# Kernel optimization log

Measured on AMD Instinct MI355X. Metric: run time of the kernel, lower is better.

The kernel has to match this reference:

```python
import jax, jax.numpy as jnp
import numpy as np

M = 4096
N = 4096

def _twiddle(L):
    k = jnp.arange(L, dtype=jnp.float32)
    ang = -np.pi * k / (2.0 * L)
    return jnp.stack([jnp.cos(ang), jnp.sin(ang)], axis=-1).astype(jnp.float32)  # [L,2] = exp(-i*pi*k/(2L))

def setup_inputs() -> dict:
    key = jax.random.key(0)
    x = jax.random.normal(key, (M, N), dtype=jnp.float32)
    return {"x": x, "expkM": _twiddle(M), "expkN": _twiddle(N)}

def reference(x, expkM, expkN):
    # 2D DCT-II via Makhoul even/odd reordering + single complex FFT2 + twiddle multiply.
    # out[u,v] = sum_{m,n} x[m,n] cos(pi*u*(2m+1)/(2M)) cos(pi*v*(2n+1)/(2N))
    Mh, Nh = x.shape
    permM = jnp.concatenate([jnp.arange(0, Mh, 2), jnp.arange(Mh - 1, 0, -2)])
    permN = jnp.concatenate([jnp.arange(0, Nh, 2), jnp.arange(Nh - 1, 0, -2)])
    y = x[permM][:, permN]                       # even/odd reorder in both dims
    Y = jnp.fft.fft2(y)                          # [M,N] complex
    wM = expkM[:, 0] + 1j * expkM[:, 1]          # exp(-i*pi*u/(2M))
    wN = expkN[:, 0] + 1j * expkN[:, 1]          # exp(-i*pi*v/(2N))
    Yrev = jnp.roll(Y[::-1, :], 1, axis=0)       # Y[(M-u) % M, v]
    C = 0.5 * (wN[None, :] * Y + jnp.conj(wN)[None, :] * jnp.conj(Yrev))
    return jnp.real(wM[:, None] * C)
```

## Files before the change

kernel.cpp:

```cpp
#include <hip/hip_runtime.h>
#include <math.h>

#define NFULL 4096
#define NH    2048
#define T     256

__device__ __forceinline__ int sw(int i) { return i ^ (((i >> 4) & 7) << 1); }

__device__ __forceinline__ float2 cmul(float2 a, float2 b) {
    return make_float2(a.x * b.x - a.y * b.y, a.x * b.y + a.y * b.x);
}

__device__ __forceinline__ float2 sc(float ang) {
    float s, c;
    __sincosf(ang, &s, &c);
    return make_float2(c, s);
}

__device__ __forceinline__ void dft8(float2 v[8]) {
    const float s = 0.70710678118654752f;
    float2 e0 = v[0], o0 = v[1], e1 = v[2], o1 = v[3];
    float2 e2 = v[4], o2 = v[5], e3 = v[6], o3 = v[7];
    float2 t0 = make_float2(e0.x + e2.x, e0.y + e2.y);
    float2 t1 = make_float2(e0.x - e2.x, e0.y - e2.y);
    float2 t2 = make_float2(e1.x + e3.x, e1.y + e3.y);
    float2 t3 = make_float2(e1.x - e3.x, e1.y - e3.y);
    float2 E0 = make_float2(t0.x + t2.x, t0.y + t2.y);
    float2 E2 = make_float2(t0.x - t2.x, t0.y - t2.y);
    float2 E1 = make_float2(t1.x + t3.y, t1.y - t3.x);
    float2 E3 = make_float2(t1.x - t3.y, t1.y + t3.x);
    float2 u0 = make_float2(o0.x + o2.x, o0.y + o2.y);
    float2 u1 = make_float2(o0.x - o2.x, o0.y - o2.y);
    float2 u2 = make_float2(o1.x + o3.x, o1.y + o3.y);
    float2 u3 = make_float2(o1.x - o3.x, o1.y - o3.y);
    float2 O0 = make_float2(u0.x + u2.x, u0.y + u2.y);
    float2 O2 = make_float2(u0.x - u2.x, u0.y - u2.y);
    float2 O1 = make_float2(u1.x + u3.y, u1.y - u3.x);
    float2 O3 = make_float2(u1.x - u3.y, u1.y + u3.x);
    O1 = make_float2(s * (O1.x + O1.y), s * (O1.y - O1.x));
    O2 = make_float2(O2.y, -O2.x);
    O3 = make_float2(s * (O3.y - O3.x), s * (-O3.x - O3.y));
    v[0] = make_float2(E0.x + O0.x, E0.y + O0.y);
    v[4] = make_float2(E0.x - O0.x, E0.y - O0.y);
    v[1] = make_float2(E1.x + O1.x, E1.y + O1.y);
    v[5] = make_float2(E1.x - O1.x, E1.y - O1.y);
    v[2] = make_float2(E2.x + O2.x, E2.y + O2.y);
    v[6] = make_float2(E2.x - O2.x, E2.y - O2.y);
    v[3] = make_float2(E3.x + O3.x, E3.y + O3.y);
    v[7] = make_float2(E3.x - O3.x, E3.y - O3.y);
}

__device__ __forceinline__ void dft4(float2 v[4]) {
    float2 t0 = make_float2(v[0].x + v[2].x, v[0].y + v[2].y);
    float2 t1 = make_float2(v[0].x - v[2].x, v[0].y - v[2].y);
    float2 t2 = make_float2(v[1].x + v[3].x, v[1].y + v[3].y);
    float2 t3 = make_float2(v[1].x - v[3].x, v[1].y - v[3].y);
    v[0] = make_float2(t0.x + t2.x, t0.y + t2.y);
    v[2] = make_float2(t0.x - t2.x, t0.y - t2.y);
    v[1] = make_float2(t1.x + t3.y, t1.y - t3.x);
    v[3] = make_float2(t1.x - t3.y, t1.y + t3.x);
}

__global__ __launch_bounds__(T, 5) void dct_rows_rfft(const float* __restrict__ in,
                                                      const float* __restrict__ expk,
                                                      float* __restrict__ out) {
    __shared__ float2 A[NH];
    __shared__ float2 B[NH];
    const int row = blockIdx.x;
    const int t = threadIdx.x;
    const float4* __restrict__ src4 = (const float4*)(in + (size_t)row * NFULL);

    float2 v[8];
    {
        float4 f0 = src4[t];
        float4 f1 = src4[t + 256];
        float4 f2 = src4[t + 512];
        float4 f3 = src4[t + 768];
        float4 g3 = src4[1023 - t];
        float4 g2 = src4[767 - t];
        float4 g1 = src4[511 - t];
        float4 g0 = src4[255 - t];
        v[0] = make_float2(f0.x, f0.z);
        v[1] = make_float2(f1.x, f1.z);
        v[2] = make_float2(f2.x, f2.z);
        v[3] = make_float2(f3.x, f3.z);
        v[4] = make_float2(g3.w, g3.y);
        v[5] = make_float2(g2.w, g2.y);
        v[6] = make_float2(g1.w, g1.y);
        v[7] = make_float2(g0.w, g0.y);
        dft8(v);
        #pragma unroll
        for (int r = 0; r < 8; ++r) B[sw(8 * t + r)] = v[r];
    }
    __syncthreads();
    {
        #pragma unroll
        for (int r = 0; r < 8; ++r) v[r] = B[sw(t + 256 * r)];
        const float a = -(float)M_PI / 32.0f * (float)(t & 7);
        float2 w1 = sc(a), w2 = sc(2.0f * a), w4 = sc(4.0f * a);
        float2 w3 = cmul(w1, w2), w5 = cmul(w1, w4), w6 = cmul(w2, w4);
        float2 w7 = cmul(w3, w4);
        v[1] = cmul(v[1], w1); v[2] = cmul(v[2], w2); v[3] = cmul(v[3], w3);
        v[4] = cmul(v[4], w4); v[5] = cmul(v[5], w5); v[6] = cmul(v[6], w6);
        v[7] = cmul(v[7], w7);
        dft8(v);
        const int d = ((t >> 3) << 6) + (t & 7);
        #pragma unroll
        for (int r = 0; r < 8; ++r) A[sw(d + 8 * r)] = v[r];
    }
    __syncthreads();
    {
        #pragma unroll
        for (int r = 0; r < 8; ++r) v[r] = A[sw(t + 256 * r)];
        const float a = -(float)M_PI / 256.0f * (float)(t & 63);
        float2 w1 = sc(a), w2 = sc(2.0f * a), w4 = sc(4.0f * a);
        float2 w3 = cmul(w1, w2), w5 = cmul(w1, w4), w6 = cmul(w2, w4);
        float2 w7 = cmul(w3, w4);
        v[1] = cmul(v[1], w1); v[2] = cmul(v[2], w2); v[3] = cmul(v[3], w3);
        v[4] = cmul(v[4], w4); v[5] = cmul(v[5], w5); v[6] = cmul(v[6], w6);
        v[7] = cmul(v[7], w7);
        dft8(v);
        const int d = ((t >> 6) << 9) + (t & 63);
        #pragma unroll
        for (int r = 0; r < 8; ++r) B[sw(d + 64 * r)] = v[r];
    }
    __syncthreads();
    #pragma unroll
    for (int h = 0; h < 2; ++h) {
        const int j = t + 256 * h;
        float2 u[4];
        #pragma unroll
        for (int r = 0; r < 4; ++r) u[r] = B[sw(j + 512 * r)];
        const float a = -(float)M_PI / 1024.0f * (float)j;
        float2 w1 = sc(a), w2 = sc(2.0f * a);
        float2 w3 = cmul(w1, w2);
        u[1] = cmul(u[1], w1);
        u[2] = cmul(u[2], w2);
        u[3] = cmul(u[3], w3);
        dft4(u);
        #pragma unroll
        for (int r = 0; r < 4; ++r) A[sw(j + 512 * r)] = u[r];
    }
    __syncthreads();

    const float2* __restrict__ ek = (const float2*)expk;
    float* __restrict__ dst = out + (size_t)row * NFULL;
    #pragma unroll
    for (int i = 0; i < 8; ++i) {
        const int k = t + T * i;
        if (k == 0) {
            float2 z0 = A[sw(0)];
            dst[0]  = ek[0].x * (z0.x + z0.y);
            dst[NH] = ek[NH].x * (z0.x - z0.y);
        } else {
            float2 Zk = A[sw(k)];
            float2 Zr = A[sw(NH - k)];
            float2 E = make_float2(0.5f * (Zk.x + Zr.x), 0.5f * (Zk.y - Zr.y));
            float2 O = make_float2(0.5f * (Zk.y + Zr.y), 0.5f * (Zr.x - Zk.x));
            float2 uu = sc(-(float)M_PI / 2048.0f * (float)k);
            float2 Y = make_float2(E.x + uu.x * O.x - uu.y * O.y,
                                   E.y + uu.x * O.y + uu.y * O.x);
            float2 wk = ek[k];
            dst[k] = wk.x * Y.x - wk.y * Y.y;
            float2 wn = ek[NFULL - k];
            dst[NFULL - k] = wn.x * Y.x + wn.y * Y.y;
        }
    }
}

__global__ __launch_bounds__(256) void transpose4k(const float* __restrict__ in,
                                                   float* __restrict__ out) {
    __shared__ float tile[32][33];
    const int x0 = blockIdx.x * 32;
    const int y0 = blockIdx.y * 32;
    const int tx = threadIdx.x & 31;
    const int ty = threadIdx.x >> 5;

    #pragma unroll
    for (int i = 0; i < 32; i += 8)
        tile[ty + i][tx] = in[(size_t)(y0 + ty + i) * NFULL + (x0 + tx)];
    __syncthreads();
    #pragma unroll
    for (int i = 0; i < 32; i += 8)
        out[(size_t)(x0 + ty + i) * NFULL + (y0 + tx)] = tile[tx][ty + i];
}

extern "C" void kernel_launch(void* const* d_in, const int* in_sizes, int n_in,
                              void* d_out, int out_size, void* d_ws, size_t ws_size,
                              hipStream_t stream) {
    const float* x     = (const float*)d_in[0];
    const float* expkM = (const float*)d_in[1];
    const float* expkN = (const float*)d_in[2];
    float* out = (float*)d_out;
    float* ws1 = (float*)d_ws;

    dct_rows_rfft<<<NFULL, T, 0, stream>>>(x, expkN, ws1);
    transpose4k<<<dim3(128, 128), 256, 0, stream>>>(ws1, out);
    dct_rows_rfft<<<NFULL, T, 0, stream>>>(out, expkM, ws1);
    transpose4k<<<dim3(128, 128), 256, 0, stream>>>(ws1, out);
}
```

Before: 113.5 us.

## Process each DCT row with a single wavefront and drop block barriers

The row DCT kernel now assigns one 64-lane wavefront per row, with two rows per 128-thread block. Each lane handles four times as many FFT butterflies, kept in registers. All __syncthreads calls are removed, relying on wavefront-level ordering of LDS accesses. A single in-place LDS buffer per row replaces the previous A/B ping-pong, halving LDS per row. The aim is to remove barrier stalls and raise per-thread ILP, at the cost of higher register pressure. It also relies on implicit intra-wave LDS ordering with no explicit fence.

```diff
diff --git a/kernel.cpp b/kernel.cpp
--- a/kernel.cpp
+++ b/kernel.cpp
@@ -3,7 +3,8 @@
 
 #define NFULL 4096
 #define NH    2048
-#define T     256
+#define ROWS_PER_BLK 2
+#define T     (64 * ROWS_PER_BLK)
 
 __device__ __forceinline__ int sw(int i) { return i ^ (((i >> 4) & 7) << 1); }
 
@@ -61,93 +62,125 @@
     v[3] = make_float2(t1.x - t3.y, t1.y + t3.x);
 }
 
-__global__ __launch_bounds__(T, 5) void dct_rows_rfft(const float* __restrict__ in,
+__global__ __launch_bounds__(T, 2) void dct_rows_wave(const float* __restrict__ in,
                                                       const float* __restrict__ expk,
                                                       float* __restrict__ out) {
-    __shared__ float2 A[NH];
-    __shared__ float2 B[NH];
-    const int row = blockIdx.x;
-    const int t = threadIdx.x;
+    __shared__ float2 L[ROWS_PER_BLK][NH];
+    const int wave = threadIdx.x >> 6;
+    const int l    = threadIdx.x & 63;
+    const int row  = ROWS_PER_BLK * blockIdx.x + wave;
+    float2* __restrict__ A = L[wave];
     const float4* __restrict__ src4 = (const float4*)(in + (size_t)row * NFULL);
 
-    float2 v[8];
+    float2 v[4][8];
+    #pragma unroll
+    for (int i = 0; i < 4; ++i) {
+        const int b = l + 64 * i;
+        float4 f0 = src4[b];
+        float4 f1 = src4[b + 256];
+        float4 f2 = src4[b + 512];
+        float4 f3 = src4[b + 768];
+        float4 g3 = src4[1023 - b];
+        float4 g2 = src4[767 - b];
+        float4 g1 = src4[511 - b];
+        float4 g0 = src4[255 - b];
+        v[i][0] = make_float2(f0.x, f0.z);
+        v[i][1] = make_float2(f1.x, f1.z);
+        v[i][2] = make_float2(f2.x, f2.z);
+        v[i][3] = make_float2(f3.x, f3.z);
+        v[i][4] = make_float2(g3.w, g3.y);
+        v[i][5] = make_float2(g2.w, g2.y);
+        v[i][6] = make_float2(g1.w, g1.y);
+        v[i][7] = make_float2(g0.w, g0.y);
+    }
+    #pragma unroll
+    for (int i = 0; i < 4; ++i) {
+        dft8(v[i]);
+        const int b = l + 64 * i;
+        #pragma unroll
+        for (int r = 0; r < 8; ++r) A[sw(8 * b + r)] = v[i][r];
+    }
+
     {
-        float4 f0 = src4[t];
-        float4 f1 = src4[t + 256];
-        float4 f2 = src4[t + 512];
-        float4 f3 = src4[t + 768];
-        float4 g3 = src4[1023 - t];
-        float4 g2 = src4[767 - t];
-        float4 g1 = src4[511 - t];
-        float4 g0 = src4[255 - t];
-        v[0] = make_float2(f0.x, f0.z);
-        v[1] = make_float2(f1.x, f1.z);
-        v[2] = make_float2(f2.x, f2.z);
-        v[3] = make_float2(f3.x, f3.z);
-        v[4] = make_float2(g3.w, g3.y);
-        v[5] = make_float2(g2.w, g2.y);
-        v[6] = make_float2(g1.w, g1.y);
-        v[7] = make_float2(g0.w, g0.y);
-        dft8(v);
-        #pragma unroll
-        for (int r = 0; r < 8; ++r) B[sw(8 * t + r)] = v[r];
-    }
-    __syncthreads();
-    {
-        #pragma unroll
-        for (int r = 0; r < 8; ++r) v[r] = B[sw(t + 256 * r)];
-        const float a = -(float)M_PI / 32.0f * (float)(t & 7);
+        #pragma unroll
+        for (int i = 0; i < 4; ++i)
+            #pragma unroll
+            for (int r = 0; r < 8; ++r) v[i][r] = A[sw(l + 64 * i + 256 * r)];
+        const float a = -(float)M_PI / 32.0f * (float)(l & 7);
         float2 w1 = sc(a), w2 = sc(2.0f * a), w4 = sc(4.0f * a);
         float2 w3 = cmul(w1, w2), w5 = cmul(w1, w4), w6 = cmul(w2, w4);
         float2 w7 = cmul(w3, w4);
-        v[1] = cmul(v[1], w1); v[2] = cmul(v[2], w2); v[3] = cmul(v[3], w3);
-        v[4] = cmul(v[4], w4); v[5] = cmul(v[5], w5); v[6] = cmul(v[6], w6);
-        v[7] = cmul(v[7], w7);
-        dft8(v);
-        const int d = ((t >> 3) << 6) + (t & 7);
-        #pragma unroll
-        for (int r = 0; r < 8; ++r) A[sw(d + 8 * r)] = v[r];
-    }
-    __syncthreads();
+        #pragma unroll
+        for (int i = 0; i < 4; ++i) {
+            v[i][1] = cmul(v[i][1], w1); v[i][2] = cmul(v[i][2], w2);
+            v[i][3] = cmul(v[i][3], w3); v[i][4] = cmul(v[i][4], w4);
+            v[i][5] = cmul(v[i][5], w5); v[i][6] = cmul(v[i][6], w6);
+            v[i][7] = cmul(v[i][7], w7);
+            dft8(v[i]);
+        }
+        #pragma unroll
+        for (int i = 0; i < 4; ++i) {
+            const int q = l + 64 * i;
+            const int d = ((q >> 3) << 6) + (q & 7);
+            #pragma unroll
+            for (int r = 0; r < 8; ++r) A[sw(d + 8 * r)] = v[i][r];
+        }
+    }
+
     {
         #pragma unroll
-        for (int r = 0; r < 8; ++r) v[r] = A[sw(t + 256 * r)];
-        const float a = -(float)M_PI / 256.0f * (float)(t & 63);
+        for (int i = 0; i < 4; ++i)
+            #pragma unroll
+            for (int r = 0; r < 8; ++r) v[i][r] = A[sw(l + 64 * i + 256 * r)];
+        const float a = -(float)M_PI / 256.0f * (float)l;
         float2 w1 = sc(a), w2 = sc(2.0f * a), w4 = sc(4.0f * a);
         float2 w3 = cmul(w1, w2), w5 = cmul(w1, w4), w6 = cmul(w2, w4);
         float2 w7 = cmul(w3, w4);
-        v[1] = cmul(v[1], w1); v[2] = cmul(v[2], w2); v[3] = cmul(v[3], w3);
-        v[4] = cmul(v[4], w4); v[5] = cmul(v[5], w5); v[6] = cmul(v[6], w6);
-        v[7] = cmul(v[7], w7);
-        dft8(v);
-        const int d = ((t >> 6) << 9) + (t & 63);
-        #pragma unroll
-        for (int r = 0; r < 8; ++r) B[sw(d + 64 * r)] = v[r];
-    }
-    __syncthreads();
-    #pragma unroll
-    for (int h = 0; h < 2; ++h) {
-        const int j = t + 256 * h;
-        float2 u[4];
-        #pragma unroll
-        for (int r = 0; r < 4; ++r) u[r] = B[sw(j + 512 * r)];
-        const float a = -(float)M_PI / 1024.0f * (float)j;
-        float2 w1 = sc(a), w2 = sc(2.0f * a);
-        float2 w3 = cmul(w1, w2);
-        u[1] = cmul(u[1], w1);
-        u[2] = cmul(u[2], w2);
-        u[3] = cmul(u[3], w3);
-        dft4(u);
-        #pragma unroll
-        for (int r = 0; r < 4; ++r) A[sw(j + 512 * r)] = u[r];
-    }
-    __syncthreads();
+        #pragma unroll
+        for (int i = 0; i < 4; ++i) {
+            v[i][1] = cmul(v[i][1], w1); v[i][2] = cmul(v[i][2], w2);
+            v[i][3] = cmul(v[i][3], w3); v[i][4] = cmul(v[i][4], w4);
+            v[i][5] = cmul(v[i][5], w5); v[i][6] = cmul(v[i][6], w6);
+            v[i][7] = cmul(v[i][7], w7);
+            dft8(v[i]);
+        }
+        #pragma unroll
+        for (int i = 0; i < 4; ++i) {
+            const int q = l + 64 * i;
+            const int d = ((q >> 6) << 9) + (q & 63);
+            #pragma unroll
+            for (int r = 0; r < 8; ++r) A[sw(d + 64 * r)] = v[i][r];
+        }
+    }
+
+    {
+        float2 u[8][4];
+        #pragma unroll
+        for (int i = 0; i < 8; ++i)
+            #pragma unroll
+            for (int r = 0; r < 4; ++r) u[i][r] = A[sw(l + 64 * i + 512 * r)];
+        #pragma unroll
+        for (int i = 0; i < 8; ++i) {
+            const int q = l + 64 * i;
+            const float a = -(float)M_PI / 1024.0f * (float)q;
+            float2 w1 = sc(a), w2 = sc(2.0f * a);
+            float2 w3 = cmul(w1, w2);
+            u[i][1] = cmul(u[i][1], w1);
+            u[i][2] = cmul(u[i][2], w2);
+            u[i][3] = cmul(u[i][3], w3);
+            dft4(u[i]);
+        }
+        #pragma unroll
+        for (int i = 0; i < 8; ++i)
+            #pragma unroll
+            for (int r = 0; r < 4; ++r) A[sw(l + 64 * i + 512 * r)] = u[i][r];
+    }
 
     const float2* __restrict__ ek = (const float2*)expk;
     float* __restrict__ dst = out + (size_t)row * NFULL;
     #pragma unroll
-    for (int i = 0; i < 8; ++i) {
-        const int k = t + T * i;
+    for (int i = 0; i < 32; ++i) {
+        const int k = l + 64 * i;
         if (k == 0) {
             float2 z0 = A[sw(0)];
             dst[0]  = ek[0].x * (z0.x + z0.y);
@@ -194,8 +227,8 @@
     float* out = (float*)d_out;
     float* ws1 = (float*)d_ws;
 
-    dct_rows_rfft<<<NFULL, T, 0, stream>>>(x, expkN, ws1);
+    dct_rows_wave<<<NFULL / ROWS_PER_BLK, T, 0, stream>>>(x, expkN, ws1);
     transpose4k<<<dim3(128, 128), 256, 0, stream>>>(ws1, out);
-    dct_rows_rfft<<<NFULL, T, 0, stream>>>(out, expkM, ws1);
+    dct_rows_wave<<<NFULL / ROWS_PER_BLK, T, 0, stream>>>(out, expkM, ws1);
     transpose4k<<<dim3(128, 128), 256, 0, stream>>>(ws1, out);
 }
```

Result: slower. 128.1 us (+12.9%).
